# Performance work log

Measured on AMD Instinct MI355X. Metric: run time of the kernel, lower is better.

The kernel has to match this reference:

```python
import jax, jax.numpy as jnp
import numpy as np
import math

B, C, H, W = 8, 512, 32, 32
NH = 8           # num_heads
G = 32           # group norm groups
EPS = 1e-6


def group_norm(x, gamma, beta, groups=G, eps=EPS):
    # x: [B, C, H, W]
    b, c, h, w = x.shape
    xr = x.reshape(b, groups, c // groups, h, w)
    mu = xr.mean(axis=(2, 3, 4), keepdims=True)
    var = xr.var(axis=(2, 3, 4), keepdims=True)
    xn = ((xr - mu) * jax.lax.rsqrt(var + eps)).reshape(b, c, h, w)
    return xn * gamma[None, :, None, None] + beta[None, :, None, None]


def conv2d(x, w, b, pad):
    y = jax.lax.conv_general_dilated(
        x, w, window_strides=(1, 1), padding=[(pad, pad), (pad, pad)],
        dimension_numbers=("NCHW", "OIHW", "NCHW"))
    return y + b[None, :, None, None]


def setup_inputs() -> dict:
    key = jax.random.key(0)
    ks = jax.random.split(key, 20)
    def n(k, shape, s=0.02):
        return jax.random.normal(k, shape, dtype=jnp.float32) * s
    f32 = jnp.float32
    return {
        "hidden_states": jax.random.normal(ks[0], (B, C, H, W), dtype=f32),
        "pre_g": jnp.ones(C, f32), "pre_b": jnp.zeros(C, f32),
        "norm_g": jnp.ones(C, f32), "norm_b": jnp.zeros(C, f32),
        "post_g": jnp.ones(C, f32), "post_b": jnp.zeros(C, f32),
        "pos_emb": n(ks[1], (1, C, 32, 32)),
        "wq": n(ks[2], (C, C)), "wk": n(ks[3], (C, C)), "wv": n(ks[4], (C, C)),
        "wq0": n(ks[5], (C // 2, C)), "wq1": n(ks[6], (C // 2, C)),
        "wk0": n(ks[7], (C // 2, C)), "wk1": n(ks[8], (C // 2, C)),
        "wv0": n(ks[9], (C // 2, C)), "wv1": n(ks[10], (C // 2, C)),
        "sa_w1": n(ks[11], (C // 8, C, 1, 1)), "sa_b1": jnp.zeros(C // 8, f32),
        "sa_w2": n(ks[12], (C // 8, C // 8, 3, 3)), "sa_b2": jnp.zeros(C // 8, f32),
        "sa_w3": n(ks[13], (1, C // 8, 1, 1)), "sa_b3": jnp.zeros(1, f32),
        "ff_w1": n(ks[14], (C, 2 * C)), "ff_b1": jnp.zeros(C, f32),
        "ff_w2": n(ks[15], (C, C)), "ff_b2": jnp.zeros(C, f32),
        "out_w": n(ks[16], (C, C)), "out_b": jnp.zeros(C, f32),
    }


def reference(hidden_states, pre_g, pre_b, norm_g, norm_b, post_g, post_b,
              pos_emb, wq, wk, wv, wq0, wq1, wk0, wk1, wv0, wv1,
              sa_w1, sa_b1, sa_w2, sa_b2, sa_w3, sa_b3,
              ff_w1, ff_b1, ff_w2, ff_b2, out_w, out_b):
    b, c, h, w = hidden_states.shape
    S = h * w
    residual = hidden_states
    x = group_norm(hidden_states, pre_g, pre_b)
    # H == W == 32: bilinear interpolation of pos_emb to its own size is identity
    x = x + pos_emb
    # conv-based sigmoid spatial gate
    s1 = jax.nn.silu(conv2d(x, sa_w1, sa_b1, 0))
    s2 = jax.nn.silu(conv2d(s1, sa_w2, sa_b2, 1))
    spatial_weights = jax.nn.sigmoid(conv2d(s2, sa_w3, sa_b3, 0))  # [B,1,H,W]
    spatial_enhanced = x * spatial_weights
    # standard attention path (self-attention: encoder states = normed tokens)
    sh = group_norm(x, norm_g, norm_b).reshape(b, c, S).transpose(0, 2, 1)  # [B,S,C]
    enc = sh
    hd = c // NH
    def split_heads(t):
        return t.reshape(b, S, NH, hd).transpose(0, 2, 1, 3)  # [B,NH,S,hd]
    qh = split_heads(sh @ wq.T)
    kh = split_heads(enc @ wk.T)
    vh = split_heads(enc @ wv.T)
    scores = jnp.einsum("bhqd,bhkd->bhqk", qh, kh) / math.sqrt(hd)
    probs = jax.nn.softmax(scores, axis=-1)
    standard_out = jnp.einsum("bhqk,bhkd->bhqd", probs, vh)
    standard_out = standard_out.transpose(0, 2, 1, 3).reshape(b, S, c)
    # multi-scale attention paths over the spatially gated features (single head)
    msh = spatial_enhanced.reshape(b, c, S).transpose(0, 2, 1)  # [B,S,C]
    parts = []
    for wqm, wkm, wvm in ((wq0, wk0, wv0), (wq1, wk1, wv1)):
        qm = msh @ wqm.T      # [B,S,C/2]
        km = enc @ wkm.T
        vm = enc @ wvm.T
        sc = jnp.einsum("bqd,bkd->bqk", qm, km) / math.sqrt(qm.shape[-1])
        parts.append(jnp.einsum("bqk,bkd->bqd", jax.nn.softmax(sc, axis=-1), vm))
    multi_out = jnp.concatenate(parts, axis=-1)            # [B,S,C]
    combined = jnp.concatenate([standard_out, multi_out], axis=-1)  # [B,S,2C]
    fused = jax.nn.silu(combined @ ff_w1.T + ff_b1) @ ff_w2.T + ff_b2  # dropout = eval
    final = fused @ out_w.T + out_b
    final = final.transpose(0, 2, 1).reshape(b, c, h, w)
    final = group_norm(final, post_g, post_b)
    return final + residual
```

## Files before the change

kernel.cpp:

```cpp
#include <hip/hip_runtime.h>

typedef unsigned short u16;
typedef unsigned long long u64;
typedef __attribute__((ext_vector_type(8))) short s8v;
typedef __attribute__((ext_vector_type(4))) short s4v;
typedef __attribute__((ext_vector_type(4))) float f4v;

#define LOG2E 1.4426950408889634f

__device__ __forceinline__ float b2f(u16 u) {
  union { unsigned u; float f; } x; x.u = ((unsigned)u) << 16; return x.f;
}
__device__ __forceinline__ u16 f2b(float f) {
  union { float f; unsigned u; } x; x.f = f;
  unsigned r = x.u + 0x7fffu + ((x.u >> 16) & 1u);
  return (u16)(r >> 16);
}
__device__ __forceinline__ unsigned cvtpk(float lo, float hi) {
  unsigned r;
  asm("v_cvt_pk_bf16_f32 %0, %1, %2" : "=v"(r) : "v"(lo), "v"(hi));
  return r;
}

#define MFMA16(a, b, c) __builtin_amdgcn_mfma_f32_16x16x32_bf16((a), (b), (c), 0, 0, 0)

__device__ __forceinline__ void gload16(const void* g, void* l) {
  __builtin_amdgcn_global_load_lds(
      (const __attribute__((address_space(1))) unsigned*)g,
      (__attribute__((address_space(3))) unsigned*)l, 16, 0, 0);
}

struct Segs {
  const float* src[14];
  int cum[15];
  float scl[14];
};

__global__ __launch_bounds__(256) void castk(Segs sg, u16* __restrict__ dst) {
  int gid = (blockIdx.x * 256 + threadIdx.x) * 4;
  if (gid >= sg.cum[14]) return;
  int s = 0;
  while (gid >= sg.cum[s + 1]) ++s;
  const float* sp = sg.src[s] + (gid - sg.cum[s]);
  float sc = sg.scl[s];
  f4v v = *(const f4v*)sp;
  s4v o;
  o[0] = (short)f2b(v[0] * sc); o[1] = (short)f2b(v[1] * sc);
  o[2] = (short)f2b(v[2] * sc); o[3] = (short)f2b(v[3] * sc);
  *(s4v*)(dst + gid) = o;
}

__global__ __launch_bounds__(256) void gn1_k(
    const float* __restrict__ hs, const float* __restrict__ pg, const float* __restrict__ pb,
    const float* __restrict__ pos, u16* __restrict__ xb,
    float* __restrict__ mu2, float* __restrict__ rs2)
{
  int bid = blockIdx.x;
  int b = bid >> 5, g = bid & 31;
  int tid = threadIdx.x, l = tid & 63, w = tid >> 6;
  const float* src = hs + ((size_t)b * 512 + g * 16) * 1024;
  const float* pp = pos + (size_t)(g * 16) * 1024;
  u16* dst = xb + ((size_t)b * 512 + g * 16) * 1024;
  f4v vals[16];
  float sum = 0.f, sq = 0.f;
#pragma unroll
  for (int i = 0; i < 16; ++i) {
    int idx = tid + i * 256;
    vals[i] = *(const f4v*)(src + (size_t)idx * 4);
    f4v v = vals[i];
    sum += v[0] + v[1] + v[2] + v[3];
    sq += v[0] * v[0] + v[1] * v[1] + v[2] * v[2] + v[3] * v[3];
  }
  __shared__ float red[8];
#pragma unroll
  for (int off = 1; off < 64; off <<= 1) { sum += __shfl_xor(sum, off); sq += __shfl_xor(sq, off); }
  if (l == 0) { red[w * 2] = sum; red[w * 2 + 1] = sq; }
  __syncthreads();
  float S = red[0] + red[2] + red[4] + red[6];
  float Q = red[1] + red[3] + red[5] + red[7];
  float mean = S * (1.f / 16384.f);
  float var = Q * (1.f / 16384.f) - mean * mean;
  float rstd = rsqrtf(var + 1e-6f);
  __syncthreads();
  float sum2 = 0.f, sq2 = 0.f;
#pragma unroll
  for (int i = 0; i < 16; ++i) {
    int idx = tid + i * 256;
    int c = idx >> 8;
    float gam = pg[g * 16 + c], bet = pb[g * 16 + c];
    f4v v = vals[i];
    f4v pe = *(const f4v*)(pp + (size_t)idx * 4);
    f4v o;
    s4v ob;
#pragma unroll
    for (int j = 0; j < 4; ++j) {
      o[j] = (v[j] - mean) * rstd * gam + bet + pe[j];
      ob[j] = (short)f2b(o[j]);
    }
    *(s4v*)(dst + (size_t)idx * 4) = ob;
    sum2 += o[0] + o[1] + o[2] + o[3];
    sq2 += o[0] * o[0] + o[1] * o[1] + o[2] * o[2] + o[3] * o[3];
  }
#pragma unroll
  for (int off = 1; off < 64; off <<= 1) { sum2 += __shfl_xor(sum2, off); sq2 += __shfl_xor(sq2, off); }
  if (l == 0) { red[w * 2] = sum2; red[w * 2 + 1] = sq2; }
  __syncthreads();
  if (tid == 0) {
    float S2 = red[0] + red[2] + red[4] + red[6];
    float Q2 = red[1] + red[3] + red[5] + red[7];
    float m2 = S2 * (1.f / 16384.f);
    float v2 = Q2 * (1.f / 16384.f) - m2 * m2;
    mu2[b * 32 + g] = m2;
    rs2[b * 32 + g] = rsqrtf(v2 + 1e-6f);
  }
}

__global__ __launch_bounds__(256) void trans_gn2(
    const u16* __restrict__ xb, const float* __restrict__ mu2, const float* __restrict__ rs2,
    const float* __restrict__ ng, const float* __restrict__ nb,
    u16* __restrict__ xt, u16* __restrict__ sh)
{
  __shared__ float lds[512 * 17];
  int st = blockIdx.x, b = blockIdx.y;
  int tid = threadIdx.x;
  const u16* xp = xb + (size_t)b * 512 * 1024 + st * 16;
#pragma unroll
  for (int i = 0; i < 4; ++i) {
    int idx = tid + i * 256;
    int c = idx >> 1, sq = (idx & 1) * 8;
    s8v v = *(const s8v*)(xp + (size_t)c * 1024 + sq);
#pragma unroll
    for (int j = 0; j < 8; ++j) lds[c * 17 + sq + j] = b2f((u16)v[j]);
  }
  __syncthreads();
  int s = tid & 15, cb0 = (tid >> 4) * 32;
  size_t token = (size_t)b * 1024 + st * 16 + s;
  float m0 = mu2[b * 32 + (cb0 >> 4)], m1 = mu2[b * 32 + (cb0 >> 4) + 1];
  float r0 = rs2[b * 32 + (cb0 >> 4)], r1 = rs2[b * 32 + (cb0 >> 4) + 1];
#pragma unroll
  for (int q = 0; q < 4; ++q) {
    s8v ox, os;
#pragma unroll
    for (int j = 0; j < 8; ++j) {
      int cj = q * 8 + j;
      int c = cb0 + cj;
      float v = lds[c * 17 + s];
      ox[j] = (short)f2b(v);
      float mm = (cj < 16) ? m0 : m1;
      float rr = (cj < 16) ? r0 : r1;
      os[j] = (short)f2b((v - mm) * rr * ng[c] + nb[c]);
    }
    *(s8v*)(xt + token * 512 + cb0 + q * 8) = ox;
    *(s8v*)(sh + token * 512 + cb0 + q * 8) = os;
  }
}

template <int BM, int BN, bool SILU, bool OUT32, bool BIAS>
__global__ __launch_bounds__(256, 2) void gemm_k(
    const u16* __restrict__ A, int lda,
    const u16* __restrict__ Bw, int ldb,
    void* __restrict__ Cp, int ldc,
    const float* __restrict__ bias, int K, int ntx)
{
  constexpr int WMT = BM / 2, WNT = BN / 2, MF = WMT / 16, NF = WNT / 16;
  __shared__ u16 Al[BM * 64];
  __shared__ u16 Bl[BN * 64];
  const int tid = threadIdx.x, l = tid & 63, w = tid >> 6;
  const int lg = l >> 4, lr = l & 15;
  const int wm = w >> 1, wn = w & 1;
  const int flat = blockIdx.x;
  const int cpx = gridDim.x >> 3;
  const int id = (flat & 7) * cpx + (flat >> 3);
  const int grp = id / (ntx * 4), rem = id % (ntx * 4);
  const int nt = rem >> 2, mt = grp * 4 + (rem & 3);
  const u16* Ag = A + (size_t)mt * BM * lda;
  const u16* Bg = Bw + (size_t)nt * BN * ldb;
  const f4v z = {0.f, 0.f, 0.f, 0.f};
  f4v acc[MF][NF];
#pragma unroll
  for (int i = 0; i < MF; ++i)
#pragma unroll
    for (int j = 0; j < NF; ++j) acc[i][j] = z;

  for (int kt = 0; kt < K; kt += 64) {
    __syncthreads();
    for (int f = tid; f < BM * 8; f += 256) {
      int row = f >> 3, g = (f & 7) ^ (row & 7);
      gload16(Ag + (size_t)row * lda + kt + g * 8, (char*)Al + f * 16);
    }
    for (int f = tid; f < BN * 8; f += 256) {
      int row = f >> 3, g = (f & 7) ^ (row & 7);
      gload16(Bg + (size_t)row * ldb + kt + g * 8, (char*)Bl + f * 16);
    }
    __syncthreads();
#pragma unroll
    for (int ks = 0; ks < 2; ++ks) {
      s8v af[MF], bf[NF];
#pragma unroll
      for (int mf = 0; mf < MF; ++mf) {
        int row = wm * WMT + mf * 16 + lr;
        af[mf] = *(const s8v*)((const char*)Al + row * 128 + (((ks * 4 + lg) ^ (row & 7)) << 4));
      }
#pragma unroll
      for (int nf = 0; nf < NF; ++nf) {
        int row = wn * WNT + nf * 16 + lr;
        bf[nf] = *(const s8v*)((const char*)Bl + row * 128 + (((ks * 4 + lg) ^ (row & 7)) << 4));
      }
#pragma unroll
      for (int mf = 0; mf < MF; ++mf)
#pragma unroll
        for (int nf = 0; nf < NF; ++nf)
          acc[mf][nf] = MFMA16(af[mf], bf[nf], acc[mf][nf]);
    }
  }
#pragma unroll
  for (int mf = 0; mf < MF; ++mf) {
    int row0 = mt * BM + wm * WMT + mf * 16 + lg * 4;
#pragma unroll
    for (int nf = 0; nf < NF; ++nf) {
      int col = nt * BN + wn * WNT + nf * 16 + lr;
      float bv = BIAS ? bias[col] : 0.f;
#pragma unroll
      for (int r = 0; r < 4; ++r) {
        float v = acc[mf][nf][r] + bv;
        if (SILU) v = v / (1.f + exp2f(-v * LOG2E));
        size_t off = (size_t)(row0 + r) * ldc + col;
        if (OUT32) ((float*)Cp)[off] = v;
        else ((u16*)Cp)[off] = f2b(v);
      }
    }
  }
}

__global__ __launch_bounds__(256) void im2col_k(const u16* __restrict__ s1t, u16* __restrict__ col) {
  int gid = blockIdx.x * 256 + threadIdx.x;
  if (gid >= 8192 * 64) return;
  int token = gid >> 6, c = gid & 63;
  int s = token & 1023, y = s >> 5, xx = s & 31;
  u16* dst = col + (size_t)token * 576 + c * 9;
#pragma unroll
  for (int dy = 0; dy < 3; ++dy)
#pragma unroll
    for (int dx = 0; dx < 3; ++dx) {
      int yy = y + dy - 1, x2 = xx + dx - 1;
      u16 v = 0;
      if (yy >= 0 && yy < 32 && x2 >= 0 && x2 < 32)
        v = s1t[(size_t)(token + (dy - 1) * 32 + (dx - 1)) * 64 + c];
      dst[dy * 3 + dx] = v;
    }
}

__global__ __launch_bounds__(256) void conv3_k(
    const u16* __restrict__ s2t, const float* __restrict__ w3,
    const float* __restrict__ b3, float* __restrict__ gate)
{
  int token = blockIdx.x * 256 + threadIdx.x;
  if (token >= 8192) return;
  float acc = b3[0];
#pragma unroll
  for (int q = 0; q < 8; ++q) {
    s8v v = *(const s8v*)(s2t + (size_t)token * 64 + q * 8);
#pragma unroll
    for (int e = 0; e < 8; ++e) acc += b2f((u16)v[e]) * w3[q * 8 + e];
  }
  gate[token] = 1.f / (1.f + exp2f(-acc * LOG2E));
}

__global__ __launch_bounds__(256) void mshk(
    const u16* __restrict__ xt, const float* __restrict__ gate, u16* __restrict__ msh)
{
  int gid = blockIdx.x * 256 + threadIdx.x;
  if (gid >= 8192 * 64) return;
  int token = gid >> 6, j = gid & 63;
  float gt = gate[token];
  s8v v = *(const s8v*)(xt + (size_t)token * 512 + j * 8);
  s8v o;
#pragma unroll
  for (int e = 0; e < 8; ++e) o[e] = (short)f2b(b2f((u16)v[e]) * gt);
  *(s8v*)(msh + (size_t)token * 512 + j * 8) = o;
}

template <int HD>
__global__ __launch_bounds__(256) void tv_k(const u16* __restrict__ proj, int col0,
                                            u16* __restrict__ out)
{
  __shared__ u16 tile[64][HD + 2];
  const int tid = threadIdx.x;
  const int kb = blockIdx.x, y = blockIdx.y;
  const int nh = 512 / HD;
  const int b = y / nh, hh = y % nh;
  const u16* src = proj + ((size_t)b * 1024 + kb * 64) * 2560 + col0 + hh * HD;
  for (int f = tid; f < 64 * HD / 8; f += 256) {
    int key = f / (HD / 8), c = f % (HD / 8);
    *(s8v*)&tile[key][c * 8] = *(const s8v*)(src + (size_t)key * 2560 + c * 8);
  }
  __syncthreads();
  u16* dst = out + (size_t)y * HD * 1024 + kb * 64;
  for (int idx = tid; idx < HD * 16; idx += 256) {
    int d = idx >> 4, a = idx & 15;
    u16 e0 = tile[a][d], e1 = tile[16 + a][d], e2 = tile[32 + a][d], e3 = tile[48 + a][d];
    u64 v = (u64)e0 | ((u64)e1 << 16) | ((u64)e2 << 32) | ((u64)e3 << 48);
    *(u64*)(dst + (size_t)d * 1024 + a * 4) = v;
  }
}

__global__ __launch_bounds__(256, 4) void attn_std(
    const u16* __restrict__ proj, const u16* __restrict__ vts, u16* __restrict__ comb)
{
  const int tid = threadIdx.x, l = tid & 63, w = tid >> 6;
  const int lg = l >> 4, lr = l & 15;
  const int flat = blockIdx.x;
  const int xcd = flat & 7, idx = flat >> 3;
  const int bh = xcd + 8 * (idx >> 4);
  const int qt = idx & 15;
  const int b = bh >> 3, h = bh & 7;
  const size_t tokb = (size_t)b * 1024;
  __shared__ u16 Kl[2][64 * 64];
  __shared__ u16 Vl[2][64 * 64];
  __shared__ u16 Pl[4][16 * 64];
  const int qr0 = qt * 64 + w * 16;
  s8v qf[2];
#pragma unroll
  for (int ks = 0; ks < 2; ++ks)
    qf[ks] = *(const s8v*)(proj + (tokb + qr0 + lr) * 2560 + h * 64 + ks * 32 + lg * 8);
  const f4v z = {0.f, 0.f, 0.f, 0.f};
  f4v acc[4];
  float lsl[4] = {0.f, 0.f, 0.f, 0.f};
#pragma unroll
  for (int r = 0; r < 4; ++r) acc[r] = z;

  const u16* gk[2];
  const u16* gv[2];
  char* lk[2];
  char* lv[2];
#pragma unroll
  for (int j = 0; j < 2; ++j) {
    int f = tid + j * 256;
    int key = f >> 3, g = (f & 7) ^ (key & 7);
    gk[j] = proj + (tokb + key) * 2560 + 512 + h * 64 + g * 8;
    int c = (f & 7) ^ (key & 7);
    gv[j] = vts + (size_t)bh * 64 * 1024 + (size_t)key * 1024 + c * 8;
    lk[j] = (char*)&Kl[0][0] + f * 16;
    lv[j] = (char*)&Vl[0][0] + f * 16;
  }

  auto stage = [&](int buf) {
#pragma unroll
    for (int j = 0; j < 2; ++j) {
      gload16(gk[j], lk[j] + buf * 8192);
      gload16(gv[j], lv[j] + buf * 8192);
    }
#pragma unroll
    for (int j = 0; j < 2; ++j) { gk[j] += 64 * 2560; gv[j] += 64; }
  };

  stage(0);
  __syncthreads();
  int cur = 0;
  for (int kt = 0; kt < 16; ++kt) {
    if (kt < 15) stage(cur ^ 1);
    f4v sf[4];
#pragma unroll
    for (int nf = 0; nf < 4; ++nf) sf[nf] = z;
#pragma unroll
    for (int ks = 0; ks < 2; ++ks) {
      s8v kfr[4];
#pragma unroll
      for (int nf = 0; nf < 4; ++nf) {
        int row = nf * 16 + lr;
        kfr[nf] = *(const s8v*)((const char*)&Kl[cur][0] + row * 128 + (((ks * 4 + lg) ^ (row & 7)) << 4));
      }
#pragma unroll
      for (int nf = 0; nf < 4; ++nf) sf[nf] = MFMA16(qf[ks], kfr[nf], sf[nf]);
    }
#pragma unroll
    for (int r = 0; r < 4; ++r) {
      float pv[4];
#pragma unroll
      for (int nf = 0; nf < 4; ++nf) pv[nf] = exp2f(sf[nf][r]);
      lsl[r] += (pv[0] + pv[1]) + (pv[2] + pv[3]);
      int q = lg * 4 + r;
      u64 pk = (u64)cvtpk(pv[0], pv[1]) | ((u64)cvtpk(pv[2], pv[3]) << 32);
      *(u64*)((char*)&Pl[w][0] + q * 128 + ((((lr >> 1) ^ (q & 7)) << 4)) + (lr & 1) * 8) = pk;
    }
#pragma unroll
    for (int ks2 = 0; ks2 < 2; ++ks2) {
      int g = ks2 * 4 + lg;
      s8v pfr = *(const s8v*)((const char*)&Pl[w][0] + lr * 128 + ((g ^ (lr & 7)) << 4));
#pragma unroll
      for (int nf = 0; nf < 4; ++nf) {
        int d = nf * 16 + lr;
        s8v vfr = *(const s8v*)((const char*)&Vl[cur][0] + d * 128 + ((g ^ (d & 7)) << 4));
        acc[nf] = MFMA16(pfr, vfr, acc[nf]);
      }
    }
    __syncthreads();
    cur ^= 1;
  }
#pragma unroll
  for (int r = 0; r < 4; ++r) {
    float t = lsl[r];
#pragma unroll
    for (int off = 1; off < 16; off <<= 1) t += __shfl_xor(t, off);
    float inv = 1.f / t;
    size_t row = tokb + qr0 + lg * 4 + r;
#pragma unroll
    for (int nf = 0; nf < 4; ++nf)
      comb[row * 1024 + h * 64 + nf * 16 + lr] = f2b(acc[nf][r] * inv);
  }
}

__global__ __launch_bounds__(256, 2) void attn_ms(
    const u16* __restrict__ proj, const u16* __restrict__ qm, const u16* __restrict__ vtm,
    u16* __restrict__ pacc, float* __restrict__ pl)
{
  const int tid = threadIdx.x, l = tid & 63, w = tid >> 6;
  const int lg = l >> 4, lr = l & 15;
  const int flat = blockIdx.x;
  const int xcd = flat & 7, idx = flat >> 3;
  const int bp = xcd + 8 * (idx >> 5);
  const int rest = idx & 31;
  const int qt = rest >> 1, ks = rest & 1;
  const int b = bp >> 1, p = bp & 1;
  const size_t tokb = (size_t)b * 1024;
  __shared__ u16 Kl[64 * 256];
  __shared__ u16 Vl[256 * 64];
  __shared__ u16 Pl[4][16 * 64];
  const int qr0 = qt * 64 + w * 16;
  s8v qf[8];
#pragma unroll
  for (int kf = 0; kf < 8; ++kf)
    qf[kf] = *(const s8v*)(qm + (tokb + qr0 + lr) * 512 + p * 256 + kf * 32 + lg * 8);
  const f4v z = {0.f, 0.f, 0.f, 0.f};
  f4v acc[16];
#pragma unroll
  for (int i = 0; i < 16; ++i) acc[i] = z;
  float lsl[4] = {0.f, 0.f, 0.f, 0.f};
  const u16* vbase = vtm + (size_t)bp * 256 * 1024;

  const u16* gk[8];
  const u16* gv[8];
#pragma unroll
  for (int j = 0; j < 8; ++j) {
    int f = tid + j * 256;
    int key = f >> 5, pgc = f & 31;
    int g = (pgc & 24) | ((pgc & 7) ^ (key & 7));
    gk[j] = proj + (tokb + ks * 512 + key) * 2560 + 1536 + p * 256 + g * 8;
    int d = f >> 3, c = (f & 7) ^ (d & 7);
    gv[j] = vbase + (size_t)d * 1024 + ks * 512 + c * 8;
  }

  for (int kk = 0; kk < 8; ++kk) {
    __syncthreads();
#pragma unroll
    for (int j = 0; j < 8; ++j) gload16(gk[j], (char*)Kl + (tid + j * 256) * 16);
#pragma unroll
    for (int j = 0; j < 8; ++j) gload16(gv[j], (char*)Vl + (tid + j * 256) * 16);
#pragma unroll
    for (int j = 0; j < 8; ++j) { gk[j] += 64 * 2560; gv[j] += 64; }
    __syncthreads();
    f4v sf[4];
#pragma unroll
    for (int nf = 0; nf < 4; ++nf) sf[nf] = z;
#pragma unroll
    for (int ksi = 0; ksi < 8; ++ksi) {
      s8v kfr[4];
#pragma unroll
      for (int nf = 0; nf < 4; ++nf) {
        int row = nf * 16 + lr;
        int g = ksi * 4 + lg;
        int pg2 = (g & 24) | ((g & 7) ^ (row & 7));
        kfr[nf] = *(const s8v*)((const char*)Kl + row * 512 + (pg2 << 4));
      }
#pragma unroll
      for (int nf = 0; nf < 4; ++nf) sf[nf] = MFMA16(qf[ksi], kfr[nf], sf[nf]);
    }
#pragma unroll
    for (int r = 0; r < 4; ++r) {
      float pv[4];
#pragma unroll
      for (int nf = 0; nf < 4; ++nf) pv[nf] = exp2f(sf[nf][r]);
      lsl[r] += (pv[0] + pv[1]) + (pv[2] + pv[3]);
      int q = lg * 4 + r;
      u64 pk = (u64)cvtpk(pv[0], pv[1]) | ((u64)cvtpk(pv[2], pv[3]) << 32);
      *(u64*)((char*)&Pl[w][0] + q * 128 + ((((lr >> 1) ^ (q & 7)) << 4)) + (lr & 1) * 8) = pk;
    }
#pragma unroll
    for (int ks2 = 0; ks2 < 2; ++ks2) {
      int g = ks2 * 4 + lg;
      s8v pfr = *(const s8v*)((const char*)&Pl[w][0] + lr * 128 + ((g ^ (lr & 7)) << 4));
#pragma unroll
      for (int nfd = 0; nfd < 16; ++nfd) {
        int d = nfd * 16 + lr;
        s8v vfr = *(const s8v*)((const char*)Vl + d * 128 + ((g ^ (d & 7)) << 4));
        acc[nfd] = MFMA16(pfr, vfr, acc[nfd]);
      }
    }
  }
#pragma unroll
  for (int r = 0; r < 4; ++r) {
    float t = lsl[r];
#pragma unroll
    for (int off = 1; off < 16; off <<= 1) t += __shfl_xor(t, off);
    size_t prow = ((size_t)(bp * 2 + ks) * 16 + qt) * 64 + w * 16 + lg * 4 + r;
#pragma unroll
    for (int nfd = 0; nfd < 16; ++nfd)
      pacc[prow * 256 + nfd * 16 + lr] = f2b(acc[nfd][r]);
    if (lr == 0) pl[prow] = t;
  }
}

__global__ __launch_bounds__(256) void ms_comb(
    const u16* __restrict__ pacc, const float* __restrict__ pl,
    u16* __restrict__ comb)
{
  const int qt = blockIdx.x, bp = blockIdx.y;
  const int tid = threadIdx.x;
  const int row = tid >> 2, seg = tid & 3;
  size_t prow0 = ((size_t)(bp * 2 + 0) * 16 + qt) * 64 + row;
  size_t prow1 = ((size_t)(bp * 2 + 1) * 16 + qt) * 64 + row;
  float inv = 1.f / (pl[prow0] + pl[prow1]);
  const int b = bp >> 1, p = bp & 1;
  size_t orow = ((size_t)b * 1024 + qt * 64 + row) * 1024 + 512 + p * 256 + seg * 64;
#pragma unroll
  for (int j = 0; j < 8; ++j) {
    s8v v0 = *(const s8v*)(pacc + prow0 * 256 + seg * 64 + j * 8);
    s8v v1 = *(const s8v*)(pacc + prow1 * 256 + seg * 64 + j * 8);
    s8v ov;
#pragma unroll
    for (int e = 0; e < 8; ++e)
      ov[e] = (short)f2b((b2f((u16)v0[e]) + b2f((u16)v1[e])) * inv);
    *(s8v*)(comb + orow + j * 8) = ov;
  }
}

__global__ __launch_bounds__(256) void gn3_stats(
    const float* __restrict__ fin, float* __restrict__ mu3, float* __restrict__ rs3)
{
  int bid = blockIdx.x;
  int b = bid >> 5, g = bid & 31;
  int tid = threadIdx.x, l = tid & 63, w = tid >> 6;
  const float* fp = fin + (size_t)b * 1024 * 512 + g * 16;
  float sum = 0.f, sq = 0.f;
#pragma unroll
  for (int i = 0; i < 16; ++i) {
    int idx = tid + i * 256;
    int s = idx >> 2, cq = idx & 3;
    f4v v = *(const f4v*)(fp + (size_t)s * 512 + cq * 4);
    sum += v[0] + v[1] + v[2] + v[3];
    sq += v[0] * v[0] + v[1] * v[1] + v[2] * v[2] + v[3] * v[3];
  }
  __shared__ float red[8];
#pragma unroll
  for (int off = 1; off < 64; off <<= 1) { sum += __shfl_xor(sum, off); sq += __shfl_xor(sq, off); }
  if (l == 0) { red[w * 2] = sum; red[w * 2 + 1] = sq; }
  __syncthreads();
  if (tid == 0) {
    float S = red[0] + red[2] + red[4] + red[6];
    float Q = red[1] + red[3] + red[5] + red[7];
    float mean = S * (1.f / 16384.f);
    float var = Q * (1.f / 16384.f) - mean * mean;
    mu3[b * 32 + g] = mean;
    rs3[b * 32 + g] = rsqrtf(var + 1e-6f);
  }
}

__global__ __launch_bounds__(256) void final_k(
    const float* __restrict__ fin, const float* __restrict__ mu3, const float* __restrict__ rs3,
    const float* __restrict__ postg, const float* __restrict__ postb,
    const float* __restrict__ res, float* __restrict__ out)
{
  __shared__ float lds[16 * 513];
  int st = blockIdx.x, b = blockIdx.y;
  int tid = threadIdx.x;
  const float* fp = fin + ((size_t)b * 1024 + st * 16) * 512;
#pragma unroll
  for (int i = 0; i < 8; ++i) {
    int idx = tid + i * 256;
    int s = idx >> 7, cq = idx & 127;
    f4v v = *(const f4v*)(fp + (size_t)s * 512 + cq * 4);
#pragma unroll
    for (int j = 0; j < 4; ++j) lds[s * 513 + cq * 4 + j] = v[j];
  }
  __syncthreads();
#pragma unroll
  for (int cc = 0; cc < 2; ++cc) {
    int c = tid * 2 + cc;
    int g = c >> 4;
    float m = mu3[b * 32 + g], rv = rs3[b * 32 + g];
    float ga = postg[c], be = postb[c];
    const float* rp = res + ((size_t)b * 512 + c) * 1024 + st * 16;
    float* op = out + ((size_t)b * 512 + c) * 1024 + st * 16;
#pragma unroll
    for (int q = 0; q < 4; ++q) {
      f4v rr = *(const f4v*)(rp + q * 4);
      f4v o;
#pragma unroll
      for (int j = 0; j < 4; ++j) {
        float v = lds[(q * 4 + j) * 513 + c];
        o[j] = (v - m) * rv * ga + be + rr[j];
      }
      *(f4v*)(op + q * 4) = o;
    }
  }
}

extern "C" void kernel_launch(void* const* d_in, const int* in_sizes, int n_in,
                              void* d_out, int out_size, void* d_ws, size_t ws_size,
                              hipStream_t stream) {
  (void)in_sizes; (void)n_in; (void)out_size; (void)ws_size;
  const float* hs     = (const float*)d_in[0];
  const float* pre_g  = (const float*)d_in[1];
  const float* pre_b  = (const float*)d_in[2];
  const float* norm_g = (const float*)d_in[3];
  const float* norm_b = (const float*)d_in[4];
  const float* post_g = (const float*)d_in[5];
  const float* post_b = (const float*)d_in[6];
  const float* pos    = (const float*)d_in[7];
  const float* sa_b1  = (const float*)d_in[18];
  const float* sa_b2  = (const float*)d_in[20];
  const float* sa_w3  = (const float*)d_in[21];
  const float* sa_b3  = (const float*)d_in[22];
  const float* ff_b1  = (const float*)d_in[24];
  const float* ff_b2  = (const float*)d_in[26];
  const float* out_b  = (const float*)d_in[28];

  char* ws = (char*)d_ws;
  size_t off = 0;
  auto alloc = [&](size_t bytes) -> void* {
    void* pp = ws + off;
    off += (bytes + 255) & ~(size_t)255;
    return pp;
  };
  float* x    = (float*)alloc((size_t)16777216);
  u16* sh     = (u16*)alloc((size_t)8388608);
  u16* xt     = (u16*)alloc((size_t)8388608);
  float* mu2  = (float*)alloc(1024);
  float* rs2  = (float*)alloc(1024);
  float* mu3  = (float*)alloc(1024);
  float* rs3  = (float*)alloc(1024);
  float* pl   = (float*)alloc(262144);
  u16* wcat   = (u16*)alloc((size_t)2691072 * 2);
  u16* proj   = (u16*)alloc((size_t)8192 * 2560 * 2);
  u16* qmb    = (u16*)alloc((size_t)8388608);
  u16* s1t    = (u16*)alloc((size_t)1048576);
  u16* colb   = (u16*)alloc((size_t)8192 * 576 * 2);
  u16* s2t    = (u16*)alloc((size_t)1048576);
  float* gate = (float*)alloc((size_t)32768);
  u16* msh    = (u16*)alloc((size_t)8388608);
  u16* comb   = (u16*)alloc((size_t)16777216);
  u16* f1     = (u16*)alloc((size_t)8388608);
  u16* f2     = (u16*)alloc((size_t)8388608);
  float* fin  = x;
  u16* xb     = (u16*)x;
  u16* pacc   = (u16*)x;
  u16* vts    = colb;
  u16* vtm    = msh;

  u16* Wbig = wcat;
  u16* Wq01 = wcat + 1310720;
  u16* W1   = wcat + 1572864;
  u16* W2   = wcat + 1605632;
  u16* Wff1 = wcat + 1642496;
  u16* Wff2 = wcat + 2166784;
  u16* Wout = wcat + 2428928;

  Segs sg;
  const int srcidx[14] = {8, 9, 10, 13, 14, 15, 16, 11, 12, 17, 19, 23, 25, 27};
  const int segsz[14] = {262144, 262144, 262144, 131072, 131072, 131072, 131072,
                         131072, 131072, 32768, 36864, 524288, 262144, 262144};
  int cum = 0;
  for (int i = 0; i < 14; ++i) {
    sg.src[i] = (const float*)d_in[srcidx[i]];
    sg.cum[i] = cum;
    sg.scl[i] = 1.f;
    cum += segsz[i];
  }
  sg.cum[14] = cum;
  sg.scl[0] = 0.125f * LOG2E;
  sg.scl[7] = 0.0625f * LOG2E;
  sg.scl[8] = 0.0625f * LOG2E;

  dim3 blk(256);
  castk<<<2628, blk, 0, stream>>>(sg, wcat);
  gn1_k<<<256, blk, 0, stream>>>(hs, pre_g, pre_b, pos, xb, mu2, rs2);
  trans_gn2<<<dim3(64, 8), blk, 0, stream>>>(xb, mu2, rs2, norm_g, norm_b, xt, sh);
  gemm_k<128, 128, false, false, false><<<1280, blk, 0, stream>>>(
      sh, 512, Wbig, 512, proj, 2560, nullptr, 512, 20);
  gemm_k<64, 64, true, false, true><<<128, blk, 0, stream>>>(
      xt, 512, W1, 512, s1t, 64, sa_b1, 512, 1);
  im2col_k<<<2048, blk, 0, stream>>>(s1t, colb);
  gemm_k<64, 64, true, false, true><<<128, blk, 0, stream>>>(
      colb, 576, W2, 576, s2t, 64, sa_b2, 576, 1);
  conv3_k<<<32, blk, 0, stream>>>(s2t, sa_w3, sa_b3, gate);
  mshk<<<2048, blk, 0, stream>>>(xt, gate, msh);
  gemm_k<128, 64, false, false, false><<<512, blk, 0, stream>>>(
      msh, 512, Wq01, 512, qmb, 512, nullptr, 512, 8);
  tv_k<64><<<dim3(16, 64), blk, 0, stream>>>(proj, 1024, vts);
  tv_k<256><<<dim3(16, 16), blk, 0, stream>>>(proj, 2048, vtm);
  attn_std<<<1024, blk, 0, stream>>>(proj, vts, comb);
  attn_ms<<<512, blk, 0, stream>>>(proj, qmb, vtm, pacc, pl);
  ms_comb<<<dim3(16, 16), blk, 0, stream>>>(pacc, pl, comb);
  gemm_k<128, 64, true, false, true><<<512, blk, 0, stream>>>(
      comb, 1024, Wff1, 1024, f1, 512, ff_b1, 1024, 8);
  gemm_k<128, 64, false, false, true><<<512, blk, 0, stream>>>(
      f1, 512, Wff2, 512, f2, 512, ff_b2, 512, 8);
  gemm_k<128, 64, false, true, true><<<512, blk, 0, stream>>>(
      f2, 512, Wout, 512, fin, 512, out_b, 512, 8);
  gn3_stats<<<256, blk, 0, stream>>>(fin, mu3, rs3);
  final_k<<<dim3(64, 8), blk, 0, stream>>>(fin, mu3, rs3, post_g, post_b, hs, (float*)d_out);
}
```

Baseline: 256.6 us.

## Fold ff_w2 into out projection and fuse gate scaling into Q GEMM

Precomputes a combined weight Wout·Wff2 and a combined bias each call, removing one full-size GEMM and the f2 intermediate. Folds the spatial gate into the multi-scale Q projection as a per-row epilogue scale, removing the separate gating kernel and its buffer. The cost is a few small setup kernels and extra bf16 rounding of the combined weight.

```diff
diff --git a/kernel.cpp b/kernel.cpp
--- a/kernel.cpp
+++ b/kernel.cpp
@@ -50,6 +50,40 @@
   *(s4v*)(dst + gid) = o;
 }
 
+__global__ __launch_bounds__(256) void tr512(const u16* __restrict__ in, u16* __restrict__ out) {
+  __shared__ u16 t[64][72];
+  const int bi = blockIdx.x & 7, bj = blockIdx.x >> 3;
+  const int tid = threadIdx.x;
+  for (int f = tid; f < 512; f += 256) {
+    int row = f >> 3, c8 = (f & 7) * 8;
+    *(s8v*)&t[row][c8] = *(const s8v*)(in + (size_t)(bj * 64 + row) * 512 + bi * 64 + c8);
+  }
+  __syncthreads();
+  for (int f = tid; f < 512; f += 256) {
+    int row = f >> 3, c8 = (f & 7) * 8;
+    s8v v;
+#pragma unroll
+    for (int j = 0; j < 8; ++j) v[j] = (short)t[c8 + j][row];
+    *(s8v*)(out + (size_t)(bi * 64 + row) * 512 + bj * 64 + c8) = v;
+  }
+}
+
+__global__ __launch_bounds__(256) void bcomb_k(
+    const float* __restrict__ Wout, const float* __restrict__ b2,
+    const float* __restrict__ ob, float* __restrict__ bc)
+{
+  int i = blockIdx.x * 256 + threadIdx.x;
+  if (i >= 512) return;
+  float s = ob[i];
+  const float* wr = Wout + (size_t)i * 512;
+  for (int j = 0; j < 512; j += 4) {
+    f4v w = *(const f4v*)(wr + j);
+    f4v b = *(const f4v*)(b2 + j);
+    s += w[0] * b[0] + w[1] * b[1] + w[2] * b[2] + w[3] * b[3];
+  }
+  bc[i] = s;
+}
+
 __global__ __launch_bounds__(256) void gn1_k(
     const float* __restrict__ hs, const float* __restrict__ pg, const float* __restrict__ pb,
     const float* __restrict__ pos, u16* __restrict__ xb,
@@ -155,12 +189,13 @@
   }
 }
 
-template <int BM, int BN, bool SILU, bool OUT32, bool BIAS>
+template <int BM, int BN, bool SILU, bool OUT32, bool BIAS, bool RSCALE>
 __global__ __launch_bounds__(256, 2) void gemm_k(
     const u16* __restrict__ A, int lda,
     const u16* __restrict__ Bw, int ldb,
     void* __restrict__ Cp, int ldc,
-    const float* __restrict__ bias, int K, int ntx)
+    const float* __restrict__ bias, int K, int ntx,
+    const float* __restrict__ rscale)
 {
   constexpr int WMT = BM / 2, WNT = BN / 2, MF = WMT / 16, NF = WNT / 16;
   __shared__ u16 Al[BM * 64];
@@ -223,6 +258,7 @@
 #pragma unroll
       for (int r = 0; r < 4; ++r) {
         float v = acc[mf][nf][r] + bv;
+        if (RSCALE) v *= rscale[row0 + r];
         if (SILU) v = v / (1.f + exp2f(-v * LOG2E));
         size_t off = (size_t)(row0 + r) * ldc + col;
         if (OUT32) ((float*)Cp)[off] = v;
@@ -264,20 +300,6 @@
     for (int e = 0; e < 8; ++e) acc += b2f((u16)v[e]) * w3[q * 8 + e];
   }
   gate[token] = 1.f / (1.f + exp2f(-acc * LOG2E));
-}
-
-__global__ __launch_bounds__(256) void mshk(
-    const u16* __restrict__ xt, const float* __restrict__ gate, u16* __restrict__ msh)
-{
-  int gid = blockIdx.x * 256 + threadIdx.x;
-  if (gid >= 8192 * 64) return;
-  int token = gid >> 6, j = gid & 63;
-  float gt = gate[token];
-  s8v v = *(const s8v*)(xt + (size_t)token * 512 + j * 8);
-  s8v o;
-#pragma unroll
-  for (int e = 0; e < 8; ++e) o[e] = (short)f2b(b2f((u16)v[e]) * gt);
-  *(s8v*)(msh + (size_t)token * 512 + j * 8) = o;
 }
 
 template <int HD>
@@ -624,6 +646,7 @@
   const float* ff_b1  = (const float*)d_in[24];
   const float* ff_b2  = (const float*)d_in[26];
   const float* out_b  = (const float*)d_in[28];
+  const float* wout_f = (const float*)d_in[27];
 
   char* ws = (char*)d_ws;
   size_t off = 0;
@@ -647,15 +670,16 @@
   u16* colb   = (u16*)alloc((size_t)8192 * 576 * 2);
   u16* s2t    = (u16*)alloc((size_t)1048576);
   float* gate = (float*)alloc((size_t)32768);
-  u16* msh    = (u16*)alloc((size_t)8388608);
+  u16* vtm    = (u16*)alloc((size_t)8388608);
   u16* comb   = (u16*)alloc((size_t)16777216);
   u16* f1     = (u16*)alloc((size_t)8388608);
-  u16* f2     = (u16*)alloc((size_t)8388608);
+  u16* wff2t  = (u16*)alloc((size_t)524288);
+  u16* wcomb  = (u16*)alloc((size_t)524288);
+  float* bcomb = (float*)alloc(2048);
   float* fin  = x;
   u16* xb     = (u16*)x;
   u16* pacc   = (u16*)x;
   u16* vts    = colb;
-  u16* vtm    = msh;
 
   u16* Wbig = wcat;
   u16* Wq01 = wcat + 1310720;
@@ -683,30 +707,32 @@
 
   dim3 blk(256);
   castk<<<2628, blk, 0, stream>>>(sg, wcat);
+  tr512<<<64, blk, 0, stream>>>(Wff2, wff2t);
+  gemm_k<128, 64, false, false, false, false><<<32, blk, 0, stream>>>(
+      Wout, 512, wff2t, 512, wcomb, 512, nullptr, 512, 8, nullptr);
+  bcomb_k<<<2, blk, 0, stream>>>(wout_f, ff_b2, out_b, bcomb);
+
   gn1_k<<<256, blk, 0, stream>>>(hs, pre_g, pre_b, pos, xb, mu2, rs2);
   trans_gn2<<<dim3(64, 8), blk, 0, stream>>>(xb, mu2, rs2, norm_g, norm_b, xt, sh);
-  gemm_k<128, 128, false, false, false><<<1280, blk, 0, stream>>>(
-      sh, 512, Wbig, 512, proj, 2560, nullptr, 512, 20);
-  gemm_k<64, 64, true, false, true><<<128, blk, 0, stream>>>(
-      xt, 512, W1, 512, s1t, 64, sa_b1, 512, 1);
+  gemm_k<128, 128, false, false, false, false><<<1280, blk, 0, stream>>>(
+      sh, 512, Wbig, 512, proj, 2560, nullptr, 512, 20, nullptr);
+  gemm_k<64, 64, true, false, true, false><<<128, blk, 0, stream>>>(
+      xt, 512, W1, 512, s1t, 64, sa_b1, 512, 1, nullptr);
   im2col_k<<<2048, blk, 0, stream>>>(s1t, colb);
-  gemm_k<64, 64, true, false, true><<<128, blk, 0, stream>>>(
-      colb, 576, W2, 576, s2t, 64, sa_b2, 576, 1);
+  gemm_k<64, 64, true, false, true, false><<<128, blk, 0, stream>>>(
+      colb, 576, W2, 576, s2t, 64, sa_b2, 576, 1, nullptr);
   conv3_k<<<32, blk, 0, stream>>>(s2t, sa_w3, sa_b3, gate);
-  mshk<<<2048, blk, 0, stream>>>(xt, gate, msh);
-  gemm_k<128, 64, false, false, false><<<512, blk, 0, stream>>>(
-      msh, 512, Wq01, 512, qmb, 512, nullptr, 512, 8);
+  gemm_k<128, 64, false, false, false, true><<<512, blk, 0, stream>>>(
+      xt, 512, Wq01, 512, qmb, 512, nullptr, 512, 8, gate);
   tv_k<64><<<dim3(16, 64), blk, 0, stream>>>(proj, 1024, vts);
   tv_k<256><<<dim3(16, 16), blk, 0, stream>>>(proj, 2048, vtm);
   attn_std<<<1024, blk, 0, stream>>>(proj, vts, comb);
   attn_ms<<<512, blk, 0, stream>>>(proj, qmb, vtm, pacc, pl);
   ms_comb<<<dim3(16, 16), blk, 0, stream>>>(pacc, pl, comb);
-  gemm_k<128, 64, true, false, true><<<512, blk, 0, stream>>>(
-      comb, 1024, Wff1, 1024, f1, 512, ff_b1, 1024, 8);
-  gemm_k<128, 64, false, false, true><<<512, blk, 0, stream>>>(
-      f1, 512, Wff2, 512, f2, 512, ff_b2, 512, 8);
-  gemm_k<128, 64, false, true, true><<<512, blk, 0, stream>>>(
-      f2, 512, Wout, 512, fin, 512, out_b, 512, 8);
+  gemm_k<128, 64, true, false, true, false><<<512, blk, 0, stream>>>(
+      comb, 1024, Wff1, 1024, f1, 512, ff_b1, 1024, 8, nullptr);
+  gemm_k<128, 64, false, true, true, false><<<512, blk, 0, stream>>>(
+      f1, 512, wcomb, 512, fin, 512, bcomb, 512, 8, nullptr);
   gn3_stats<<<256, blk, 0, stream>>>(fin, mu3, rs3);
   final_k<<<dim3(64, 8), blk, 0, stream>>>(fin, mu3, rs3, post_g, post_b, hs, (float*)d_out);
 }
```

Result: slower. 268.9 us (+4.8%).
